# Kernel optimization log

Measured on AMD Instinct MI355X. Metric: run time of the kernel, lower is better.

Reference implementation:

```python
import jax, jax.numpy as jnp
import numpy as np

D = 512      # input_size == per-head embed_size (wide attention)
H = 8        # num_attn_heads


def setup_inputs() -> dict:
    key = jax.random.key(0)
    ks = jax.random.split(key, 8)
    B, S = 2, 2048
    scale = 1.0 / np.sqrt(D)
    return {
        "Xin_q": jax.random.normal(ks[0], (B, S, D), dtype=jnp.float32),
        "Xin_k": jax.random.normal(ks[1], (B, S, D), dtype=jnp.float32),
        "Xin_v": jax.random.normal(ks[2], (B, S, D), dtype=jnp.float32),
        # per-head projection weights, stored as [H, D_in, D_out] (bias-free)
        "Wq": jax.random.normal(ks[3], (H, D, D), dtype=jnp.float32) * scale,
        "Wk": jax.random.normal(ks[4], (H, D, D), dtype=jnp.float32) * scale,
        "Wv": jax.random.normal(ks[5], (H, D, D), dtype=jnp.float32) * scale,
        # output projection: concat(H*D) -> D, with bias
        "Wz": jax.random.normal(ks[6], (H * D, D), dtype=jnp.float32) * (1.0 / np.sqrt(H * D)),
        "bz": jax.random.normal(ks[7], (D,), dtype=jnp.float32) * 0.01,
    }


def reference(Xin_q, Xin_k, Xin_v, Wq, Wk, Wv, Wz, bz):
    B, Sq, _ = Xin_q.shape
    inv4 = 1.0 / (D ** 0.25)  # each of Q and K scaled by embed_size**(1/4)
    # project all heads at once: [B,H,S,D]
    q = jnp.einsum("bsd,hde->bhse", Xin_q, Wq) * inv4
    k = jnp.einsum("bsd,hde->bhse", Xin_k, Wk) * inv4
    v = jnp.einsum("bsd,hde->bhse", Xin_v, Wv)
    attn = jax.nn.softmax(jnp.einsum("bhqe,bhke->bhqk", q, k), axis=-1)
    z = jnp.einsum("bhqk,bhke->bhqe", attn, v)        # [B,H,S,D]
    # concat heads along last dim (head-major order matches torch.cat over the head loop)
    z = jnp.transpose(z, (0, 2, 1, 3)).reshape(B, Sq, H * D)
    out = z @ Wz + bz                                  # [B,S,D]
    attn_avg = jnp.mean(attn, axis=1)                  # [B,Sq,Skv]
    return out, attn_avg
```

## Files before the change

### kernel.cpp

```cpp
#include <hip/hip_runtime.h>
#include <math.h>

#define BB 2
#define SS 2048
#define D_ 512
#define H_ 8
#define MS (BB * SS)
#define HD (H_ * D_)

typedef short bf16x8 __attribute__((ext_vector_type(8)));
typedef float f32x4 __attribute__((ext_vector_type(4)));

__device__ inline unsigned short f2bf(float f) {
    union { float f; unsigned u; } x{f};
    unsigned r = x.u + 0x7fff + ((x.u >> 16) & 1);
    return (unsigned short)(r >> 16);
}
__device__ inline float bf2f(unsigned short u) {
    union { unsigned u; float f; } x{(unsigned)u << 16};
    return x.f;
}

constexpr size_t SZ_X   = (size_t)MS * D_ * 2;
constexpr size_t SZ_W   = (size_t)H_ * D_ * D_ * 2;
constexpr size_t SZ_WZ  = (size_t)HD * D_ * 2;
constexpr size_t SZ_QK  = (size_t)H_ * MS * D_ * 2;
constexpr size_t SZ_SC  = (size_t)H_ * BB * SS * SS * 2;
constexpr size_t SZ_Z   = (size_t)MS * HD * 2;
constexpr size_t SZ_OP  = (size_t)2 * MS * D_ * 4;
constexpr size_t SZ_LV  = (size_t)H_ * BB * SS * 4;
constexpr size_t OFF_XQ  = 0;
constexpr size_t OFF_XK  = OFF_XQ + SZ_X;
constexpr size_t OFF_XV  = OFF_XK + SZ_X;
constexpr size_t OFF_WQT = OFF_XV + SZ_X;
constexpr size_t OFF_WKT = OFF_WQT + SZ_W;
constexpr size_t OFF_WVT = OFF_WKT + SZ_W;
constexpr size_t OFF_WZT = OFF_WVT + SZ_W;
constexpr size_t OFF_QB  = OFF_WZT + SZ_WZ;
constexpr size_t OFF_KB  = OFF_QB + SZ_QK;
constexpr size_t OFF_VT  = OFF_KB + SZ_QK;
constexpr size_t OFF_SC  = OFF_VT + SZ_QK;
constexpr size_t OFF_Z   = OFF_SC + SZ_SC;
constexpr size_t OFF_OP  = OFF_Z + SZ_Z;
constexpr size_t OFF_LV  = OFF_OP + SZ_OP;
constexpr size_t WS_TOTAL = OFF_LV + SZ_LV;
__device__ __align__(256) unsigned char g_ws[WS_TOTAL];

__device__ inline void gl2lds16(const unsigned short* g, unsigned short* l) {
    __builtin_amdgcn_global_load_lds(
        (const __attribute__((address_space(1))) void*)g,
        (__attribute__((address_space(3))) void*)l, 16, 0, 0);
}

__global__ __launch_bounds__(256) void gemm_bt_k(
    const unsigned short* __restrict__ A, const unsigned short* __restrict__ B,
    void* __restrict__ Cv, int K, int ldA, int ldB, int ldC,
    long sA1, long sA2, long sB1, long sB2, long sC1, long sC2, int d2,
    float alpha, const float* __restrict__ bias, int outBf16, int doExp,
    const float* __restrict__ rowScale, long sR1, long sR2)
{
    __shared__ unsigned short As[128 * 64];
    __shared__ unsigned short Bs[128 * 64];
    const int gx = gridDim.x, gy = gridDim.y, gz = gridDim.z;
    int bx, by, bz;
    if (((gy * gz) & 7) == 0) {
        const long L = blockIdx.x + (long)gx * (blockIdx.y + (long)gy * blockIdx.z);
        const int d = (int)(L & 7);
        const long s = L >> 3;
        bx = (int)(s % gx);
        const long yz = d + 8 * (s / gx);
        by = (int)(yz % gy);
        bz = (int)(yz / gy);
    } else {
        bx = blockIdx.x; by = blockIdx.y; bz = blockIdx.z;
    }
    const int z1 = bz / d2, z2 = bz % d2;
    A += z1 * sA1 + z2 * sA2;
    B += z1 * sB1 + z2 * sB2;
    const long cOff = z1 * sC1 + z2 * sC2;
    const long rsOff = z1 * sR1 + z2 * sR2;
    const int m0 = by * 128, n0 = bx * 128;
    const int tid = threadIdx.x;
    const int w = tid >> 6, l = tid & 63;

    const int sr = l >> 3;
    const int sq = (l & 7) ^ sr;
    const unsigned short* ga = A + (long)(m0 + w * 32 + sr) * ldA + sq * 8;
    const unsigned short* gb = B + (long)(n0 + w * 32 + sr) * ldB + sq * 8;
    unsigned short* laA = As + w * 2048;
    unsigned short* laB = Bs + w * 2048;

    const int wm = w >> 1, wn = w & 1;
    const int q = l >> 4;
    const int sl = l & 7;
    const int mA = wm * 64 + (l & 15);
    const int nB = wn * 64 + (l & 15);
    const int s0 = ((q) ^ sl) * 8;
    const int s1 = ((q + 4) ^ sl) * 8;
    const unsigned short* pa0 = As + mA * 64 + s0;
    const unsigned short* pa1 = As + mA * 64 + s1;
    const unsigned short* pb0 = Bs + nB * 64 + s0;
    const unsigned short* pb1 = Bs + nB * 64 + s1;

    f32x4 acc[4][4] = {};
    for (int kk = 0; kk < K; kk += 64) {
#pragma unroll
        for (int i = 0; i < 4; i++) {
            gl2lds16(ga + (long)i * 8 * ldA, laA + i * 512);
            gl2lds16(gb + (long)i * 8 * ldB, laB + i * 512);
        }
        ga += 64; gb += 64;
        __syncthreads();
        bf16x8 af[4], bf[4];
#pragma unroll
        for (int i = 0; i < 4; i++) {
            af[i] = *(const bf16x8*)(pa0 + i * 1024);
            bf[i] = *(const bf16x8*)(pb0 + i * 1024);
        }
#pragma unroll
        for (int mi = 0; mi < 4; mi++)
#pragma unroll
            for (int ni = 0; ni < 4; ni++)
                acc[mi][ni] = __builtin_amdgcn_mfma_f32_16x16x32_bf16(
                    af[mi], bf[ni], acc[mi][ni], 0, 0, 0);
#pragma unroll
        for (int i = 0; i < 4; i++) {
            af[i] = *(const bf16x8*)(pa1 + i * 1024);
            bf[i] = *(const bf16x8*)(pb1 + i * 1024);
        }
#pragma unroll
        for (int mi = 0; mi < 4; mi++)
#pragma unroll
            for (int ni = 0; ni < 4; ni++)
                acc[mi][ni] = __builtin_amdgcn_mfma_f32_16x16x32_bf16(
                    af[mi], bf[ni], acc[mi][ni], 0, 0, 0);
        __syncthreads();
    }

    const int rowB = m0 + wm * 64 + q * 4;
    const int colB = n0 + wn * 64 + (l & 15);
    if (outBf16) {
        unsigned short* C = (unsigned short*)Cv + cOff;
#pragma unroll
        for (int mi = 0; mi < 4; mi++) {
#pragma unroll
            for (int rg = 0; rg < 4; rg++) {
                const int row = rowB + mi * 16 + rg;
                const float rs = rowScale ? rowScale[rsOff + row] : 1.0f;
#pragma unroll
                for (int ni = 0; ni < 4; ni++) {
                    float v = alpha * acc[mi][ni][rg];
                    if (doExp) v = __expf(v);
                    C[(long)row * ldC + colB + ni * 16] = f2bf(v * rs);
                }
            }
        }
    } else {
        float* C = (float*)Cv + cOff;
#pragma unroll
        for (int ni = 0; ni < 4; ni++) {
            const int col = colB + ni * 16;
            const float bs = bias ? bias[col] : 0.f;
#pragma unroll
            for (int mi = 0; mi < 4; mi++)
#pragma unroll
                for (int rg = 0; rg < 4; rg++)
                    C[(long)(rowB + mi * 16 + rg) * ldC + col] =
                        alpha * acc[mi][ni][rg] + bs;
        }
    }
}

__global__ __launch_bounds__(256) void cvt3_k(
    const float* __restrict__ i0, const float* __restrict__ i1, const float* __restrict__ i2,
    unsigned short* __restrict__ o0, unsigned short* __restrict__ o1,
    unsigned short* __restrict__ o2, long n4)
{
    const float* in = blockIdx.z == 0 ? i0 : (blockIdx.z == 1 ? i1 : i2);
    unsigned short* out = blockIdx.z == 0 ? o0 : (blockIdx.z == 1 ? o1 : o2);
    long i = (long)blockIdx.x * 256 + threadIdx.x;
    if (i >= n4) return;
    float4 v = ((const float4*)in)[i];
    ushort4 o;
    o.x = f2bf(v.x); o.y = f2bf(v.y); o.z = f2bf(v.z); o.w = f2bf(v.w);
    ((ushort4*)out)[i] = o;
}

__global__ __launch_bounds__(256) void transcvt3_k(
    const float* __restrict__ i0, const float* __restrict__ i1, const float* __restrict__ i2,
    unsigned short* __restrict__ o0, unsigned short* __restrict__ o1,
    unsigned short* __restrict__ o2)
{
    __shared__ float t[32][33];
    const int zt = blockIdx.z >> 3, h = blockIdx.z & 7;
    const float* in = (zt == 0 ? i0 : (zt == 1 ? i1 : i2)) + (long)h * D_ * D_;
    unsigned short* out = (zt == 0 ? o0 : (zt == 1 ? o1 : o2)) + (long)h * D_ * D_;
    const int r0 = blockIdx.y * 32, c0 = blockIdx.x * 32;
    const int tr = threadIdx.x >> 5, tc = threadIdx.x & 31;
#pragma unroll
    for (int i = 0; i < 4; i++)
        t[tr + i * 8][tc] = in[(long)(r0 + tr + i * 8) * D_ + c0 + tc];
    __syncthreads();
#pragma unroll
    for (int i = 0; i < 4; i++)
        out[(long)(c0 + tr + i * 8) * D_ + r0 + tc] = f2bf(t[tc][tr + i * 8]);
}

__global__ __launch_bounds__(256) void transcvt_k(
    const float* __restrict__ in, unsigned short* __restrict__ out, int R, int C)
{
    __shared__ float t[32][33];
    const int r0 = blockIdx.y * 32, c0 = blockIdx.x * 32;
    const int tr = threadIdx.x >> 5, tc = threadIdx.x & 31;
#pragma unroll
    for (int i = 0; i < 4; i++)
        t[tr + i * 8][tc] = in[(long)(r0 + tr + i * 8) * C + c0 + tc];
    __syncthreads();
#pragma unroll
    for (int i = 0; i < 4; i++)
        out[(long)(c0 + tr + i * 8) * R + r0 + tc] = f2bf(t[tc][tr + i * 8]);
}

__device__ inline float wred_sum(float v) {
#pragma unroll
    for (int o = 32; o; o >>= 1) v += __shfl_down(v, o);
    return v;
}
__global__ __launch_bounds__(256) void sumavg_k(
    const unsigned short* __restrict__ E, float* __restrict__ avg,
    float* __restrict__ linv)
{
    const int blk = blockIdx.x;
    const int b = blk >> 11, s = blk & (SS - 1);
    const int tid = threadIdx.x;
    __shared__ float red[4];
    float av[8] = {};
    const int t0 = tid * 8;
    for (int h = 0; h < H_; h++) {
        const long rowOff = ((long)(h * BB + b) * SS + s) * SS + t0;
        const ushort4 u0 = *(const ushort4*)(E + rowOff);
        const ushort4 u1 = *(const ushort4*)(E + rowOff + 4);
        float vals[8] = {bf2f(u0.x), bf2f(u0.y), bf2f(u0.z), bf2f(u0.w),
                         bf2f(u1.x), bf2f(u1.y), bf2f(u1.z), bf2f(u1.w)};
        float sum = 0.f;
#pragma unroll
        for (int i = 0; i < 8; i++) sum += vals[i];
        float wsum = wred_sum(sum);
        if ((tid & 63) == 0) red[tid >> 6] = wsum;
        __syncthreads();
        sum = red[0] + red[1] + red[2] + red[3];
        __syncthreads();
        const float inv = 1.0f / sum;
        if (tid == 0) linv[(long)(h * BB + b) * SS + s] = inv;
        const float invH = inv * 0.125f;
#pragma unroll
        for (int i = 0; i < 8; i++) av[i] += vals[i] * invH;
    }
    const long aOff = ((long)b * SS + s) * SS + t0;
    float4 a0 = {av[0], av[1], av[2], av[3]};
    float4 a1 = {av[4], av[5], av[6], av[7]};
    *(float4*)(avg + aOff) = a0;
    *(float4*)(avg + aOff + 4) = a1;
}

__global__ __launch_bounds__(256) void addbias_k(
    const float* __restrict__ p0, const float* __restrict__ p1,
    const float* __restrict__ bz, float* __restrict__ out)
{
    const long n4 = (long)MS * D_ / 4;
    long i = (long)blockIdx.x * 256 + threadIdx.x;
    if (i >= n4) return;
    const int col4 = (int)((i * 4) & (D_ - 1));
    float4 a = ((const float4*)p0)[i];
    float4 b = ((const float4*)p1)[i];
    float4 c = *(const float4*)(bz + col4);
    float4 o = {a.x + b.x + c.x, a.y + b.y + c.y, a.z + b.z + c.z, a.w + b.w + c.w};
    ((float4*)out)[i] = o;
}

extern "C" void kernel_launch(void* const* d_in, const int* in_sizes, int n_in,
                              void* d_out, int out_size, void* d_ws, size_t ws_size,
                              hipStream_t stream)
{
    const float* Xq = (const float*)d_in[0];
    const float* Xk = (const float*)d_in[1];
    const float* Xv = (const float*)d_in[2];
    const float* Wq = (const float*)d_in[3];
    const float* Wk = (const float*)d_in[4];
    const float* Wv = (const float*)d_in[5];
    const float* Wz = (const float*)d_in[6];
    const float* bz = (const float*)d_in[7];

    float* out      = (float*)d_out;
    float* attn_avg = out + (long)MS * D_;

    unsigned char* ws = nullptr;
    (void)hipGetSymbolAddress((void**)&ws, HIP_SYMBOL(g_ws));
    unsigned short* Xbq = (unsigned short*)(ws + OFF_XQ);
    unsigned short* Xbk = (unsigned short*)(ws + OFF_XK);
    unsigned short* Xbv = (unsigned short*)(ws + OFF_XV);
    unsigned short* Wqt = (unsigned short*)(ws + OFF_WQT);
    unsigned short* Wkt = (unsigned short*)(ws + OFF_WKT);
    unsigned short* Wvt = (unsigned short*)(ws + OFF_WVT);
    unsigned short* Wzt = (unsigned short*)(ws + OFF_WZT);
    unsigned short* qb  = (unsigned short*)(ws + OFF_QB);
    unsigned short* vT  = (unsigned short*)(ws + OFF_VT);
    unsigned short* scb = (unsigned short*)(ws + OFF_SC);
    unsigned short* zal = (unsigned short*)(ws + OFF_Z);
    float*          opp = (float*)(ws + OFF_OP);
    float*          linv = (float*)(ws + OFF_LV);

    const float inv4 = 1.0f / powf((float)D_, 0.25f);

    const long n4x = (long)MS * D_ / 4;
    cvt3_k<<<dim3((n4x + 255) / 256, 1, 3), 256, 0, stream>>>(
        Xq, Xk, Xv, Xbq, Xbk, Xbv, n4x);
    transcvt3_k<<<dim3(16, 16, 24), 256, 0, stream>>>(Wq, Wk, Wv, Wqt, Wkt, Wvt);
    transcvt_k<<<dim3(16, 128, 1), 256, 0, stream>>>(Wz, Wzt, HD, D_);

    gemm_bt_k<<<dim3(4, 32, 16), 256, 0, stream>>>(
        Xbq, Wqt, qb, D_, D_, D_, D_,
        (long)MS * D_, 0, (long)H_ * D_ * D_, (long)D_ * D_,
        (long)H_ * MS * D_, (long)MS * D_, 8, inv4, nullptr, 1, 0, nullptr, 0, 0);
    gemm_bt_k<<<dim3(16, 4, 16), 256, 0, stream>>>(
        Wvt, Xbv, vT, D_, D_, D_, SS,
        (long)D_ * D_, 0, 0, (long)SS * D_, (long)2 * D_ * SS, (long)D_ * SS, 2,
        1.0f, nullptr, 1, 0, nullptr, 0, 0);

    gemm_bt_k<<<dim3(16, 16, 16), 256, 0, stream>>>(
        qb, qb + (long)H_ * MS * D_, scb, D_, D_, D_, SS,
        (long)MS * D_, (long)SS * D_, (long)MS * D_, (long)SS * D_,
        (long)2 * SS * SS, (long)SS * SS, 2, 1.0f, nullptr, 1, 1, nullptr, 0, 0);

    sumavg_k<<<dim3(BB * SS), 256, 0, stream>>>(scb, attn_avg, linv);

    gemm_bt_k<<<dim3(4, 16, 16), 256, 0, stream>>>(
        scb, vT, zal, SS, SS, SS, HD,
        (long)2 * SS * SS, (long)SS * SS, (long)2 * D_ * SS, (long)D_ * SS,
        512, (long)SS * HD, 2, 1.0f, nullptr, 1, 0,
        linv, (long)BB * SS, (long)SS);

    gemm_bt_k<<<dim3(4, 32, 2), 256, 0, stream>>>(
        zal, Wzt, opp, HD / 2, HD, HD, D_,
        0, 2048, 0, 2048, 0, (long)MS * D_, 2, 1.0f, nullptr, 0, 0, nullptr, 0, 0);
    const long n4o = (long)MS * D_ / 4;
    addbias_k<<<dim3((n4o + 255) / 256), 256, 0, stream>>>(
        opp, opp + (long)MS * D_, bz, out);
}
```

Measured before the change: 512.7 us.

## Add 256x128-tile triple-buffered bf16 GEMM kernel for projections and attention

Adds a new 512-thread GEMM kernel with a 256x128 output tile, a three-stage LDS ring buffer filled by direct global-to-LDS loads, and split half-stage prefetch interleaved with MFMA phases under raised wave priority. The Q/K projection, V projection, score and PV GEMMs now launch this kernel with half as many blocks along M. The larger tile is meant to raise data reuse per block, and the deeper pipeline is meant to hide global load latency. In exchange it uses more LDS (144 KB) and more registers per block, so occupancy drops, and there are fewer blocks to fill the CUs.

```diff
diff --git a/kernel.cpp b/kernel.cpp
--- a/kernel.cpp
+++ b/kernel.cpp
@@ -52,6 +52,144 @@
         (__attribute__((address_space(3))) void*)l, 16, 0, 0);
 }
 
+__global__ __launch_bounds__(512) void gemm256_k(
+    const unsigned short* __restrict__ A, const unsigned short* __restrict__ B,
+    unsigned short* __restrict__ C, int K, int ldA, int ldB, int ldC,
+    long sA1, long sA2, long sB1, long sB2, long sC1, long sC2, int d2,
+    float alpha, int doExp, const float* __restrict__ rowScale, long sR1, long sR2)
+{
+    __shared__ unsigned short As[3][256 * 64];
+    __shared__ unsigned short Bs[3][128 * 64];
+    const int gx = gridDim.x, gy = gridDim.y, gz = gridDim.z;
+    int bx, by, bz;
+    if (((gy * gz) & 7) == 0) {
+        const long L = blockIdx.x + (long)gx * (blockIdx.y + (long)gy * blockIdx.z);
+        const int d = (int)(L & 7);
+        const long s = L >> 3;
+        bx = (int)(s % gx);
+        const long yz = d + 8 * (s / gx);
+        by = (int)(yz % gy);
+        bz = (int)(yz / gy);
+    } else {
+        bx = blockIdx.x; by = blockIdx.y; bz = blockIdx.z;
+    }
+    const int z1 = bz / d2, z2 = bz % d2;
+    A += z1 * sA1 + z2 * sA2;
+    B += z1 * sB1 + z2 * sB2;
+    const long cOff = z1 * sC1 + z2 * sC2;
+    const long rsOff = z1 * sR1 + z2 * sR2;
+    const int m0 = by * 256, n0 = bx * 128;
+    const int tid = threadIdx.x;
+    const int w = tid >> 6, l = tid & 63;
+
+    const int sr = l >> 3;
+    const int sq = (l & 7) ^ sr;
+    const unsigned short* gA = A + (long)(m0 + w * 32 + sr) * ldA + sq * 8;
+    const unsigned short* gB = B + (long)(n0 + w * 16 + sr) * ldB + sq * 8;
+
+    const int wm = w >> 1, wn = w & 1;
+    const int q = l >> 4, sl = l & 7;
+    const int mA = wm * 64 + (l & 15);
+    const int nB = wn * 64 + (l & 15);
+    const int o0 = ((q)     ^ sl) * 8;
+    const int o1 = ((q + 4) ^ sl) * 8;
+
+    const int nK = K >> 6;
+    f32x4 acc[4][4] = {};
+
+    auto STAGE = [&](int t, int h) {
+        const int s = t % 3;
+        unsigned short* lA = &As[s][0] + w * 2048;
+        unsigned short* lB = &Bs[s][0] + w * 1024;
+        const unsigned short* ga = gA + (long)t * 64;
+        const unsigned short* gb = gB + (long)t * 64;
+        if (h == 0) {
+            gl2lds16(ga,                     lA);
+            gl2lds16(ga + (long)8 * ldA,     lA + 512);
+            gl2lds16(gb,                     lB);
+        } else {
+            gl2lds16(ga + (long)16 * ldA,    lA + 1024);
+            gl2lds16(ga + (long)24 * ldA,    lA + 1536);
+            gl2lds16(gb + (long)8 * ldB,     lB + 512);
+        }
+    };
+
+    STAGE(0, 0); STAGE(0, 1);
+    STAGE(1, 0); STAGE(1, 1);
+    asm volatile("s_waitcnt vmcnt(6)" ::: "memory");
+    __builtin_amdgcn_s_barrier();
+
+    for (int t = 0; t < nK; ++t) {
+        const int s = t % 3;
+        const unsigned short* pa = &As[s][0] + mA * 64;
+        const unsigned short* pb = &Bs[s][0] + nB * 64;
+        bf16x8 bf0[4], bf1[4], af0[2], af1[2];
+
+        if (t + 2 < nK) STAGE(t + 2, 0);
+#pragma unroll
+        for (int ni = 0; ni < 4; ni++) {
+            bf0[ni] = *(const bf16x8*)(pb + ni * 1024 + o0);
+            bf1[ni] = *(const bf16x8*)(pb + ni * 1024 + o1);
+        }
+        af0[0] = *(const bf16x8*)(pa + o0);
+        af1[0] = *(const bf16x8*)(pa + o1);
+        af0[1] = *(const bf16x8*)(pa + 1024 + o0);
+        af1[1] = *(const bf16x8*)(pa + 1024 + o1);
+        __builtin_amdgcn_s_barrier();
+        __builtin_amdgcn_s_setprio(1);
+#pragma unroll
+        for (int mi = 0; mi < 2; mi++)
+#pragma unroll
+            for (int ni = 0; ni < 4; ni++) {
+                acc[mi][ni] = __builtin_amdgcn_mfma_f32_16x16x32_bf16(
+                    af0[mi], bf0[ni], acc[mi][ni], 0, 0, 0);
+                acc[mi][ni] = __builtin_amdgcn_mfma_f32_16x16x32_bf16(
+                    af1[mi], bf1[ni], acc[mi][ni], 0, 0, 0);
+            }
+        __builtin_amdgcn_s_setprio(0);
+        __builtin_amdgcn_s_barrier();
+
+        if (t + 2 < nK) STAGE(t + 2, 1);
+        af0[0] = *(const bf16x8*)(pa + 2048 + o0);
+        af1[0] = *(const bf16x8*)(pa + 2048 + o1);
+        af0[1] = *(const bf16x8*)(pa + 3072 + o0);
+        af1[1] = *(const bf16x8*)(pa + 3072 + o1);
+        __builtin_amdgcn_s_barrier();
+        __builtin_amdgcn_s_setprio(1);
+#pragma unroll
+        for (int mi = 0; mi < 2; mi++)
+#pragma unroll
+            for (int ni = 0; ni < 4; ni++) {
+                acc[2 + mi][ni] = __builtin_amdgcn_mfma_f32_16x16x32_bf16(
+                    af0[mi], bf0[ni], acc[2 + mi][ni], 0, 0, 0);
+                acc[2 + mi][ni] = __builtin_amdgcn_mfma_f32_16x16x32_bf16(
+                    af1[mi], bf1[ni], acc[2 + mi][ni], 0, 0, 0);
+            }
+        __builtin_amdgcn_s_setprio(0);
+        if (t + 2 < nK) asm volatile("s_waitcnt vmcnt(6)" ::: "memory");
+        else            asm volatile("s_waitcnt vmcnt(0)" ::: "memory");
+        __builtin_amdgcn_s_barrier();
+    }
+
+    const int rowB = m0 + wm * 64 + q * 4;
+    const int colB = n0 + wn * 64 + (l & 15);
+    unsigned short* Cp = C + cOff;
+#pragma unroll
+    for (int mi = 0; mi < 4; mi++) {
+#pragma unroll
+        for (int rg = 0; rg < 4; rg++) {
+            const int row = rowB + mi * 16 + rg;
+            const float rs = rowScale ? rowScale[rsOff + row] : 1.0f;
+#pragma unroll
+            for (int ni = 0; ni < 4; ni++) {
+                float v = alpha * acc[mi][ni][rg];
+                if (doExp) v = __expf(v);
+                Cp[(long)row * ldC + colB + ni * 16] = f2bf(v * rs);
+            }
+        }
+    }
+}
+
 __global__ __launch_bounds__(256) void gemm_bt_k(
     const unsigned short* __restrict__ A, const unsigned short* __restrict__ B,
     void* __restrict__ Cv, int K, int ldA, int ldB, int ldC,
@@ -318,26 +456,26 @@
     transcvt3_k<<<dim3(16, 16, 24), 256, 0, stream>>>(Wq, Wk, Wv, Wqt, Wkt, Wvt);
     transcvt_k<<<dim3(16, 128, 1), 256, 0, stream>>>(Wz, Wzt, HD, D_);
 
-    gemm_bt_k<<<dim3(4, 32, 16), 256, 0, stream>>>(
+    gemm256_k<<<dim3(4, 16, 16), 512, 0, stream>>>(
         Xbq, Wqt, qb, D_, D_, D_, D_,
         (long)MS * D_, 0, (long)H_ * D_ * D_, (long)D_ * D_,
-        (long)H_ * MS * D_, (long)MS * D_, 8, inv4, nullptr, 1, 0, nullptr, 0, 0);
-    gemm_bt_k<<<dim3(16, 4, 16), 256, 0, stream>>>(
+        (long)H_ * MS * D_, (long)MS * D_, 8, inv4, 0, nullptr, 0, 0);
+    gemm256_k<<<dim3(16, 2, 16), 512, 0, stream>>>(
         Wvt, Xbv, vT, D_, D_, D_, SS,
         (long)D_ * D_, 0, 0, (long)SS * D_, (long)2 * D_ * SS, (long)D_ * SS, 2,
-        1.0f, nullptr, 1, 0, nullptr, 0, 0);
-
-    gemm_bt_k<<<dim3(16, 16, 16), 256, 0, stream>>>(
+        1.0f, 0, nullptr, 0, 0);
+
+    gemm256_k<<<dim3(16, 8, 16), 512, 0, stream>>>(
         qb, qb + (long)H_ * MS * D_, scb, D_, D_, D_, SS,
         (long)MS * D_, (long)SS * D_, (long)MS * D_, (long)SS * D_,
-        (long)2 * SS * SS, (long)SS * SS, 2, 1.0f, nullptr, 1, 1, nullptr, 0, 0);
+        (long)2 * SS * SS, (long)SS * SS, 2, 1.0f, 1, nullptr, 0, 0);
 
     sumavg_k<<<dim3(BB * SS), 256, 0, stream>>>(scb, attn_avg, linv);
 
-    gemm_bt_k<<<dim3(4, 16, 16), 256, 0, stream>>>(
+    gemm256_k<<<dim3(4, 8, 16), 512, 0, stream>>>(
         scb, vT, zal, SS, SS, SS, HD,
         (long)2 * SS * SS, (long)SS * SS, (long)2 * D_ * SS, (long)D_ * SS,
-        512, (long)SS * HD, 2, 1.0f, nullptr, 1, 0,
+        512, (long)SS * HD, 2, 1.0f, 0,
         linv, (long)BB * SS, (long)SS);
 
     gemm_bt_k<<<dim3(4, 32, 2), 256, 0, stream>>>(
```

Result: slower. 618.9 us (+20.7%).

## Add 256x256-tile double-buffered GEMM kernel for projection and attention matmuls

Applied to the files above, without the earlier changes.

Adds a new 512-thread GEMM kernel with 256x256 output tiles, double-buffered LDS fed by global_load_lds, swizzled LDS reads, and an interleaved schedule that splits MFMA work into quadrants. It uses s_setprio and barriers to overlap loads with compute. The Q/K projection, V projection, QK^T score and attn*V GEMMs now use it in place of the 128-tile kernel. The goal is more data reuse per tile and better latency hiding. In exchange it needs much more LDS and registers, and small grids such as the V projection with 256 blocks may underfill the GPU.

```diff
diff --git a/kernel.cpp b/kernel.cpp
--- a/kernel.cpp
+++ b/kernel.cpp
@@ -52,6 +52,160 @@
         (__attribute__((address_space(3))) void*)l, 16, 0, 0);
 }
 
+#define BAR() __builtin_amdgcn_s_barrier()
+#define PRIO1() __builtin_amdgcn_s_setprio(1)
+#define PRIO0() __builtin_amdgcn_s_setprio(0)
+#define VMW4() asm volatile("s_waitcnt vmcnt(4)" ::: "memory")
+#define VMW0() asm volatile("s_waitcnt vmcnt(0)" ::: "memory")
+
+__device__ __forceinline__ void rd_a(const unsigned short* p, int qm, int o0, int o1,
+                                     bf16x8 (&Af)[8]) {
+#pragma unroll
+    for (int fi = 0; fi < 4; fi++) {
+        Af[2 * fi]     = *(const bf16x8*)(p + (qm * 64 + fi * 16) * 64 + o0);
+        Af[2 * fi + 1] = *(const bf16x8*)(p + (qm * 64 + fi * 16) * 64 + o1);
+    }
+}
+__device__ __forceinline__ void rd_b(const unsigned short* p, int qn, int o0, int o1,
+                                     bf16x8 (&Bf)[4]) {
+#pragma unroll
+    for (int fj = 0; fj < 2; fj++) {
+        Bf[2 * fj]     = *(const bf16x8*)(p + (qn * 32 + fj * 16) * 64 + o0);
+        Bf[2 * fj + 1] = *(const bf16x8*)(p + (qn * 32 + fj * 16) * 64 + o1);
+    }
+}
+__device__ __forceinline__ void mma_q(int qm, int qn, const bf16x8 (&Af)[8],
+                                      const bf16x8 (&Bf)[4], f32x4 (&acc)[8][4]) {
+#pragma unroll
+    for (int fi = 0; fi < 4; fi++)
+#pragma unroll
+        for (int fj = 0; fj < 2; fj++) {
+            acc[qm * 4 + fi][qn * 2 + fj] = __builtin_amdgcn_mfma_f32_16x16x32_bf16(
+                Af[2 * fi], Bf[2 * fj], acc[qm * 4 + fi][qn * 2 + fj], 0, 0, 0);
+            acc[qm * 4 + fi][qn * 2 + fj] = __builtin_amdgcn_mfma_f32_16x16x32_bf16(
+                Af[2 * fi + 1], Bf[2 * fj + 1], acc[qm * 4 + fi][qn * 2 + fj], 0, 0, 0);
+        }
+}
+
+__global__ __launch_bounds__(512, 2) void gemm256_k(
+    const unsigned short* __restrict__ A, const unsigned short* __restrict__ B,
+    unsigned short* __restrict__ C, int K, int ldA, int ldB, int ldC,
+    long sA1, long sA2, long sB1, long sB2, long sC1, long sC2, int d2,
+    float alpha, int doExp, const float* __restrict__ rowScale, long sR1, long sR2)
+{
+    __shared__ unsigned short LA[2][256 * 64];
+    __shared__ unsigned short LB[2][256 * 64];
+    const int gx = gridDim.x, gy = gridDim.y, gz = gridDim.z;
+    int bx, by, bz;
+    if (((gy * gz) & 7) == 0) {
+        const long L = blockIdx.x + (long)gx * (blockIdx.y + (long)gy * blockIdx.z);
+        const int d = (int)(L & 7);
+        const long s = L >> 3;
+        bx = (int)(s % gx);
+        const long yz = d + 8 * (s / gx);
+        by = (int)(yz % gy);
+        bz = (int)(yz / gy);
+    } else {
+        bx = blockIdx.x; by = blockIdx.y; bz = blockIdx.z;
+    }
+    const int z1 = bz / d2, z2 = bz % d2;
+    A += z1 * sA1 + z2 * sA2;
+    B += z1 * sB1 + z2 * sB2;
+    const long cOff = z1 * sC1 + z2 * sC2;
+    const long rsOff = z1 * sR1 + z2 * sR2;
+    const int m0 = by * 256, n0 = bx * 256;
+    const int tid = threadIdx.x;
+    const int w = tid >> 6, l = tid & 63;
+    const int wm = w >> 2, wn = w & 3;
+
+    const int sr = l >> 3;
+    const int sq = (l & 7) ^ sr;
+    const unsigned short* gA = A + (long)(m0 + w * 16 + sr) * ldA + sq * 8;
+    const unsigned short* gB = B + (long)(n0 + w * 16 + sr) * ldB + sq * 8;
+
+    const int q = l >> 4, sl = l & 7;
+    const int o0 = (q ^ sl) * 8;
+    const int o1 = ((q + 4) ^ sl) * 8;
+    const unsigned short* pa0 = &LA[0][(wm * 128 + (l & 15)) * 64];
+    const unsigned short* pa1 = &LA[1][(wm * 128 + (l & 15)) * 64];
+    const unsigned short* pb0 = &LB[0][(wn * 64 + (l & 15)) * 64];
+    const unsigned short* pb1 = &LB[1][(wn * 64 + (l & 15)) * 64];
+
+    const int nK2 = K >> 7;
+    f32x4 acc[8][4] = {};
+    bf16x8 Af[8], Bf0[4], Bf1[4];
+
+#define STG_A(bufi, half, t) do { \
+    gl2lds16(gA + (long)((half) * 128) * ldA + (long)(t) * 64, \
+             &LA[bufi][((half) * 128 + w * 16) * 64]); \
+    gl2lds16(gA + (long)((half) * 128 + 8) * ldA + (long)(t) * 64, \
+             &LA[bufi][((half) * 128 + w * 16 + 8) * 64]); } while (0)
+#define STG_B(bufi, half, t) do { \
+    gl2lds16(gB + (long)((half) * 128) * ldB + (long)(t) * 64, \
+             &LB[bufi][((half) * 128 + w * 16) * 64]); \
+    gl2lds16(gB + (long)((half) * 128 + 8) * ldB + (long)(t) * 64, \
+             &LB[bufi][((half) * 128 + w * 16 + 8) * 64]); } while (0)
+
+    STG_A(0, 0, 0); STG_A(0, 1, 0);
+    STG_B(0, 0, 0); STG_B(0, 1, 0);
+    STG_B(1, 0, 1); STG_B(1, 1, 1);
+    VMW4();
+    BAR();
+
+    for (int u = 0; u < nK2; ++u) {
+        const int t1 = 2 * u + 1, t2 = 2 * u + 2, t3 = 2 * u + 3;
+        const bool have = (u + 1 < nK2);
+        rd_a(pa0, 0, o0, o1, Af);
+        rd_b(pb0, 0, o0, o1, Bf0);
+        STG_A(1, 0, t1);
+        BAR(); PRIO1(); mma_q(0, 0, Af, Bf0, acc); PRIO0(); BAR();
+        rd_b(pb0, 1, o0, o1, Bf1);
+        STG_A(1, 1, t1);
+        BAR(); PRIO1(); mma_q(0, 1, Af, Bf1, acc); PRIO0(); BAR();
+        rd_a(pa0, 1, o0, o1, Af);
+        if (have) STG_B(0, 0, t2);
+        BAR(); PRIO1(); mma_q(1, 1, Af, Bf1, acc); PRIO0(); BAR();
+        if (have) STG_B(0, 1, t2);
+        BAR(); PRIO1(); mma_q(1, 0, Af, Bf0, acc); PRIO0();
+        if (have) VMW4(); else VMW0();
+        BAR();
+        rd_a(pa1, 0, o0, o1, Af);
+        rd_b(pb1, 0, o0, o1, Bf0);
+        if (have) STG_A(0, 0, t2);
+        BAR(); PRIO1(); mma_q(0, 0, Af, Bf0, acc); PRIO0(); BAR();
+        rd_b(pb1, 1, o0, o1, Bf1);
+        if (have) STG_A(0, 1, t2);
+        BAR(); PRIO1(); mma_q(0, 1, Af, Bf1, acc); PRIO0(); BAR();
+        rd_a(pa1, 1, o0, o1, Af);
+        if (have) STG_B(1, 0, t3);
+        BAR(); PRIO1(); mma_q(1, 1, Af, Bf1, acc); PRIO0(); BAR();
+        if (have) STG_B(1, 1, t3);
+        BAR(); PRIO1(); mma_q(1, 0, Af, Bf0, acc); PRIO0();
+        if (have) VMW4(); else VMW0();
+        BAR();
+    }
+#undef STG_A
+#undef STG_B
+
+    const int rowB = m0 + wm * 128 + q * 4;
+    const int colB = n0 + wn * 64 + (l & 15);
+    unsigned short* Cp = C + cOff;
+#pragma unroll
+    for (int mi = 0; mi < 8; mi++) {
+#pragma unroll
+        for (int rg = 0; rg < 4; rg++) {
+            const int row = rowB + mi * 16 + rg;
+            const float rs = rowScale ? rowScale[rsOff + row] : 1.0f;
+#pragma unroll
+            for (int nj = 0; nj < 4; nj++) {
+                float v = alpha * acc[mi][nj][rg];
+                if (doExp) v = __expf(v);
+                Cp[(long)row * ldC + colB + nj * 16] = f2bf(v * rs);
+            }
+        }
+    }
+}
+
 __global__ __launch_bounds__(256) void gemm_bt_k(
     const unsigned short* __restrict__ A, const unsigned short* __restrict__ B,
     void* __restrict__ Cv, int K, int ldA, int ldB, int ldC,
@@ -318,26 +472,26 @@
     transcvt3_k<<<dim3(16, 16, 24), 256, 0, stream>>>(Wq, Wk, Wv, Wqt, Wkt, Wvt);
     transcvt_k<<<dim3(16, 128, 1), 256, 0, stream>>>(Wz, Wzt, HD, D_);
 
-    gemm_bt_k<<<dim3(4, 32, 16), 256, 0, stream>>>(
+    gemm256_k<<<dim3(2, 16, 16), 512, 0, stream>>>(
         Xbq, Wqt, qb, D_, D_, D_, D_,
         (long)MS * D_, 0, (long)H_ * D_ * D_, (long)D_ * D_,
-        (long)H_ * MS * D_, (long)MS * D_, 8, inv4, nullptr, 1, 0, nullptr, 0, 0);
-    gemm_bt_k<<<dim3(16, 4, 16), 256, 0, stream>>>(
+        (long)H_ * MS * D_, (long)MS * D_, 8, inv4, 0, nullptr, 0, 0);
+    gemm256_k<<<dim3(8, 2, 16), 512, 0, stream>>>(
         Wvt, Xbv, vT, D_, D_, D_, SS,
         (long)D_ * D_, 0, 0, (long)SS * D_, (long)2 * D_ * SS, (long)D_ * SS, 2,
-        1.0f, nullptr, 1, 0, nullptr, 0, 0);
-
-    gemm_bt_k<<<dim3(16, 16, 16), 256, 0, stream>>>(
+        1.0f, 0, nullptr, 0, 0);
+
+    gemm256_k<<<dim3(8, 8, 16), 512, 0, stream>>>(
         qb, qb + (long)H_ * MS * D_, scb, D_, D_, D_, SS,
         (long)MS * D_, (long)SS * D_, (long)MS * D_, (long)SS * D_,
-        (long)2 * SS * SS, (long)SS * SS, 2, 1.0f, nullptr, 1, 1, nullptr, 0, 0);
+        (long)2 * SS * SS, (long)SS * SS, 2, 1.0f, 1, nullptr, 0, 0);
 
     sumavg_k<<<dim3(BB * SS), 256, 0, stream>>>(scb, attn_avg, linv);
 
-    gemm_bt_k<<<dim3(4, 16, 16), 256, 0, stream>>>(
+    gemm256_k<<<dim3(2, 8, 16), 512, 0, stream>>>(
         scb, vT, zal, SS, SS, SS, HD,
         (long)2 * SS * SS, (long)SS * SS, (long)2 * D_ * SS, (long)D_ * SS,
-        512, (long)SS * HD, 2, 1.0f, nullptr, 1, 0,
+        512, (long)SS * HD, 2, 1.0f, 0,
         linv, (long)BB * SS, (long)SS);
 
     gemm_bt_k<<<dim3(4, 32, 2), 256, 0, stream>>>(
```

After: 476.1 us. 7.1% less time.
